# Kernel optimization log

Hardware: AMD Instinct MI355X
Metric: run time of the kernel (lower is better)

Reference implementation:

```python
import jax, jax.numpy as jnp
import numpy as np

SEQ, B, D_IN, D_H = 512, 64, 512, 512


def setup_inputs() -> dict:
    key = jax.random.key(0)
    ks = jax.random.split(key, 5)
    s = 1.0 / np.sqrt(D_IN + D_H)
    inp = {
        "inputs": jax.random.normal(ks[0], (SEQ, B, D_IN), dtype=jnp.float32),
        "W_f": jax.random.normal(ks[1], (D_H, D_IN + D_H), dtype=jnp.float32) * s,
        "b_f": jnp.zeros((D_H,), jnp.float32),
        "W_i": jax.random.normal(ks[2], (D_H, D_IN + D_H), dtype=jnp.float32) * s,
        "b_i": jnp.zeros((D_H,), jnp.float32),
        "W_g": jax.random.normal(ks[3], (D_H, D_IN + D_H), dtype=jnp.float32) * s,
        "b_g": jnp.zeros((D_H,), jnp.float32),
        "W_o": jax.random.normal(ks[4], (D_H, D_IN + D_H), dtype=jnp.float32) * s,
        "b_o": jnp.zeros((D_H,), jnp.float32),
    }
    return inp


def reference(inputs, W_f, b_f, W_i, b_i, W_g, b_g, W_o, b_o):
    # inputs: [seq, batch, d_in]; states start at zeros (module default)
    B_ = inputs.shape[1]
    h0 = jnp.zeros((B_, D_H), inputs.dtype)
    c0 = jnp.zeros((B_, D_H), inputs.dtype)

    def step(carry, x_t):
        hx, cx = carry
        combined = jnp.concatenate([x_t, hx], axis=1)  # [B, d_in+d_h]
        f = jax.nn.sigmoid(combined @ W_f.T + b_f)
        i = jax.nn.sigmoid(combined @ W_i.T + b_i)
        g = jnp.tanh(combined @ W_g.T + b_g)
        o = jax.nn.sigmoid(combined @ W_o.T + b_o)
        cx = f * cx + i * g
        hx = o * jnp.tanh(cx)
        return (hx, cx), hx

    (hx, cx), stacked = jax.lax.scan(step, (h0, c0), inputs)
    return stacked, hx, cx
```

## Files before the change

kernel.cpp:

```cpp
#include <hip/hip_runtime.h>

#define SEQ   512
#define BATCH 64
#define DIN   512
#define DH    512
#define KTOT  1024
#define NWG   128
#define NTH   256
#define HBUF_BYTES 65536

#define FLAGS_BYTES 65536
#define HBASE_OFF   65536
#define XBF_OFF     (HBASE_OFF + 512 * HBUF_BYTES)
#define XBF_BYTES   ((size_t)SEQ * 4 * 16 * 1024)
#define WS_MODE1    ((size_t)HBASE_OFF + 511 * HBUF_BYTES)
#define WS_MODE2    ((size_t)XBF_OFF + XBF_BYTES)
#define FLAG_STRIDE 1

typedef __attribute__((ext_vector_type(8))) short short8;
typedef __attribute__((ext_vector_type(4))) float f32x4;

__device__ __forceinline__ float tanh_fast(float v) {
    const float e = __expf(2.0f * v);
    return 1.0f - 2.0f / (e + 1.0f);
}

__device__ __forceinline__ unsigned int f2bf(float f) {
    unsigned int u = __float_as_uint(f);
    return (u + 0x7fffu + ((u >> 16) & 1u)) >> 16;
}

__device__ __forceinline__ short8 cvt8(float4 lo, float4 hi) {
    short8 r;
    r[0] = (short)f2bf(lo.x); r[1] = (short)f2bf(lo.y);
    r[2] = (short)f2bf(lo.z); r[3] = (short)f2bf(lo.w);
    r[4] = (short)f2bf(hi.x); r[5] = (short)f2bf(hi.y);
    r[6] = (short)f2bf(hi.z); r[7] = (short)f2bf(hi.w);
    return r;
}

__device__ __forceinline__ unsigned int ld_flag(const unsigned int* p) {
    return __hip_atomic_load(p, __ATOMIC_RELAXED, __HIP_MEMORY_SCOPE_AGENT);
}
__device__ __forceinline__ void st_flag(unsigned int* p, unsigned int v) {
    __hip_atomic_store(p, v, __ATOMIC_RELAXED, __HIP_MEMORY_SCOPE_AGENT);
}
__device__ __forceinline__ unsigned long long ld_h_sc1(const unsigned long long* p) {
    return __hip_atomic_load(p, __ATOMIC_RELAXED, __HIP_MEMORY_SCOPE_AGENT);
}
__device__ __forceinline__ void st_h(unsigned long long* p, unsigned long long v) {
    __hip_atomic_store(p, v, __ATOMIC_RELAXED, __HIP_MEMORY_SCOPE_AGENT);
}

__global__ __launch_bounds__(256)
void xconv(const float* __restrict__ x, unsigned short* __restrict__ xbf)
{
    const int gid = blockIdx.x * 256 + threadIdx.x;
    const int l   = gid & 63;
    const int kt  = (gid >> 6) & 15;
    const int mtt = (gid >> 10) & 3;
    const int t   = gid >> 12;
    const float* src = x + ((size_t)t * BATCH + mtt * 16 + (l & 15)) * DIN
                         + kt * 32 + (l >> 4) * 8;
    *(short8*)(xbf + (size_t)gid * 8) =
        cvt8(*(const float4*)src, *(const float4*)(src + 4));
}

template <int MODE>
__global__ __launch_bounds__(NTH, 1)
void lstm_mfma(const float* __restrict__ x,
               const unsigned short* __restrict__ xbf,
               const float* __restrict__ Wf, const float* __restrict__ bfp,
               const float* __restrict__ Wi, const float* __restrict__ bip,
               const float* __restrict__ Wg, const float* __restrict__ bgp,
               const float* __restrict__ Wo, const float* __restrict__ bop,
               float* __restrict__ out,
               unsigned int* __restrict__ ws_u32)
{
    const int tid = threadIdx.x;
    const int l   = tid & 63;
    const int mt  = tid >> 6;
    const int wg  = blockIdx.x;
    const int j0  = wg * 4;

    const int n    = l & 15;
    const int khi  = l >> 4;
    const bool isg = (khi == 2);

    unsigned int* const flags = ws_u32;
    char* const hbase = (char*)ws_u32 + HBASE_OFF;

    const float* Wn = (n < 8) ? ((n < 4) ? Wf : Wi) : ((n < 12) ? Wg : Wo);
    const float* wrow = Wn + (size_t)(j0 + (n & 3)) * KTOT + khi * 8;
    short8 Bfr[32];
    #pragma unroll
    for (int kt = 0; kt < 32; ++kt) {
        Bfr[kt] = cvt8(*(const float4*)(wrow + kt * 32),
                       *(const float4*)(wrow + kt * 32 + 4));
    }
    const float* bptr = (khi == 0) ? bfp : (khi == 1) ? bip : (khi == 2) ? bgp : bop;
    const float4 bias4 = *(const float4*)(bptr + j0);

    float cst0 = 0.f, cst1 = 0.f, cst2 = 0.f, cst3 = 0.f;

    float* const hx_out = out + (size_t)SEQ * BATCH * DH;
    float* const cx_out = hx_out + (size_t)BATCH * DH;

    const int kth         = wg >> 3;
    const int lane_f_base = ((wg & 7) >> 1) << 4;
    const int half8       = (wg & 1) * 8;

    const unsigned int* const f0p = flags + ((size_t)mt * 128 + l) * FLAG_STRIDE;
    const unsigned int* const f1p = f0p + (size_t)64 * FLAG_STRIDE;
    unsigned int* const my_flag = flags + ((size_t)mt * 128 + wg) * FLAG_STRIDE;

    const float*  xrow_base = x + (size_t)(mt * 16 + (l & 15)) * DIN + khi * 8;
    const short8* xbf_base  = (const short8*)xbf + (size_t)mt * 16 * 64 + l;

    for (int t = 0; t < SEQ; ++t) {
        f32x4 acc_a = {0.f, 0.f, 0.f, 0.f};
        f32x4 acc_b = {0.f, 0.f, 0.f, 0.f};

        if (MODE == 2) {
            const short8* xp = xbf_base + (size_t)t * 4096;
            #pragma unroll
            for (int kt = 0; kt < 16; kt += 2) {
                acc_a = __builtin_amdgcn_mfma_f32_16x16x32_bf16(Bfr[kt], xp[kt * 64],
                                                                acc_a, 0, 0, 0);
                acc_b = __builtin_amdgcn_mfma_f32_16x16x32_bf16(Bfr[kt + 1], xp[(kt + 1) * 64],
                                                                acc_b, 0, 0, 0);
            }
        } else {
            const float* xr = xrow_base + (size_t)t * BATCH * DIN;
            #pragma unroll
            for (int kt = 0; kt < 16; kt += 2) {
                const short8 a0 = cvt8(*(const float4*)(xr + kt * 32),
                                       *(const float4*)(xr + kt * 32 + 4));
                const short8 a1 = cvt8(*(const float4*)(xr + (kt + 1) * 32),
                                       *(const float4*)(xr + (kt + 1) * 32 + 4));
                acc_a = __builtin_amdgcn_mfma_f32_16x16x32_bf16(Bfr[kt], a0, acc_a, 0, 0, 0);
                acc_b = __builtin_amdgcn_mfma_f32_16x16x32_bf16(Bfr[kt + 1], a1, acc_b, 0, 0, 0);
            }
        }

        if (t > 0) {
            const unsigned int target = (unsigned int)t;
            for (;;) {
                const unsigned int fa = ld_flag(f0p);
                const unsigned int fb = ld_flag(f1p);
                if (__all(fa >= target && fb >= target)) break;
                __builtin_amdgcn_s_sleep(1);
            }
            asm volatile("" ::: "memory");

            if (MODE == 0) {
                const unsigned long long* hp =
                    (const unsigned long long*)(hbase + ((t & 1) ^ 1) * HBUF_BYTES)
                    + ((size_t)(mt * 16) * 64 + l) * 2;
                #pragma unroll
                for (int kt = 0; kt < 16; kt += 2) {
                    union { unsigned long long u[2]; short8 v; } U0, U1;
                    U0.u[0] = ld_h_sc1(hp + kt * 128);
                    U0.u[1] = ld_h_sc1(hp + kt * 128 + 1);
                    U1.u[0] = ld_h_sc1(hp + (kt + 1) * 128);
                    U1.u[1] = ld_h_sc1(hp + (kt + 1) * 128 + 1);
                    acc_a = __builtin_amdgcn_mfma_f32_16x16x32_bf16(Bfr[16 + kt], U0.v,
                                                                    acc_a, 0, 0, 0);
                    acc_b = __builtin_amdgcn_mfma_f32_16x16x32_bf16(Bfr[17 + kt], U1.v,
                                                                    acc_b, 0, 0, 0);
                }
            } else {
                const uint4* hp = (const uint4*)(hbase + (size_t)(t - 1) * HBUF_BYTES)
                                  + ((size_t)(mt * 16) * 64 + l);
                uint4 hv[16];
                #pragma unroll
                for (int kt = 0; kt < 16; ++kt) hv[kt] = hp[kt * 64];
                #pragma unroll
                for (int kt = 0; kt < 16; kt += 2) {
                    union { uint4 u; short8 v; } U0, U1;
                    U0.u = hv[kt]; U1.u = hv[kt + 1];
                    acc_a = __builtin_amdgcn_mfma_f32_16x16x32_bf16(Bfr[16 + kt], U0.v,
                                                                    acc_a, 0, 0, 0);
                    acc_b = __builtin_amdgcn_mfma_f32_16x16x32_bf16(Bfr[17 + kt], U1.v,
                                                                    acc_b, 0, 0, 0);
                }
            }
        }

        float aq0, aq1, aq2, aq3;
        {
            const float m = isg ? 2.0f : 1.0f;
            const float p0 = acc_a[0] + acc_b[0] + bias4.x;
            const float p1 = acc_a[1] + acc_b[1] + bias4.y;
            const float p2 = acc_a[2] + acc_b[2] + bias4.z;
            const float p3 = acc_a[3] + acc_b[3] + bias4.w;
            const float y0 = 1.0f / (1.0f + __expf(-m * p0));
            const float y1 = 1.0f / (1.0f + __expf(-m * p1));
            const float y2 = 1.0f / (1.0f + __expf(-m * p2));
            const float y3 = 1.0f / (1.0f + __expf(-m * p3));
            aq0 = isg ? 2.0f * y0 - 1.0f : y0;
            aq1 = isg ? 2.0f * y1 - 1.0f : y1;
            aq2 = isg ? 2.0f * y2 - 1.0f : y2;
            aq3 = isg ? 2.0f * y3 - 1.0f : y3;
        }
        const float i0 = __shfl_xor(aq0, 16), g0 = __shfl_xor(aq0, 32), o0 = __shfl_xor(aq0, 48);
        const float i1 = __shfl_xor(aq1, 16), g1 = __shfl_xor(aq1, 32), o1 = __shfl_xor(aq1, 48);
        const float i2 = __shfl_xor(aq2, 16), g2 = __shfl_xor(aq2, 32), o2 = __shfl_xor(aq2, 48);
        const float i3 = __shfl_xor(aq3, 16), g3 = __shfl_xor(aq3, 32), o3 = __shfl_xor(aq3, 48);

        const bool active = (l < 16);
        float hq0 = 0.f, hq1 = 0.f, hq2 = 0.f, hq3 = 0.f;

        if (active) {
            cst0 = fmaf(aq0, cst0, i0 * g0); hq0 = o0 * tanh_fast(cst0);
            cst1 = fmaf(aq1, cst1, i1 * g1); hq1 = o1 * tanh_fast(cst1);
            cst2 = fmaf(aq2, cst2, i2 * g2); hq2 = o2 * tanh_fast(cst2);
            cst3 = fmaf(aq3, cst3, i3 * g3); hq3 = o3 * tanh_fast(cst3);

            if (t < SEQ - 1) {
                const unsigned long long pk =
                    (unsigned long long)(f2bf(hq0) | (f2bf(hq1) << 16))
                    | ((unsigned long long)(f2bf(hq2) | (f2bf(hq3) << 16)) << 32);
                char* const wb = (MODE == 0) ? hbase + (t & 1) * HBUF_BYTES
                                             : hbase + (size_t)t * HBUF_BYTES;
                unsigned long long* hp_w = (unsigned long long*)
                    (wb + (((size_t)(mt * 16 + kth) * 64
                            + (lane_f_base | l)) << 4) + half8);
                st_h(hp_w, pk);
            }
        }

        if (t < SEQ - 1) {
            asm volatile("s_waitcnt vmcnt(0)" ::: "memory");
            if (l == 0) st_flag(my_flag, (unsigned int)(t + 1));
        }

        if (active) {
            const int b = mt * 16 + l;
            const float4 ov = make_float4(hq0, hq1, hq2, hq3);
            *(float4*)(out + ((size_t)t * BATCH + b) * DH + j0) = ov;
            if (t == SEQ - 1) {
                *(float4*)(hx_out + (size_t)b * DH + j0) = ov;
                *(float4*)(cx_out + (size_t)b * DH + j0) =
                    make_float4(cst0, cst1, cst2, cst3);
            }
        }
    }
}

extern "C" void kernel_launch(void* const* d_in, const int* in_sizes, int n_in,
                              void* d_out, int out_size, void* d_ws, size_t ws_size,
                              hipStream_t stream)
{
    const float* x  = (const float*)d_in[0];
    const float* Wf = (const float*)d_in[1];
    const float* bf = (const float*)d_in[2];
    const float* Wi = (const float*)d_in[3];
    const float* bi = (const float*)d_in[4];
    const float* Wg = (const float*)d_in[5];
    const float* bg = (const float*)d_in[6];
    const float* Wo = (const float*)d_in[7];
    const float* bo = (const float*)d_in[8];
    float* out = (float*)d_out;

    hipMemsetAsync(d_ws, 0, FLAGS_BYTES, stream);

    unsigned int* wsp = (unsigned int*)d_ws;
    if (ws_size >= WS_MODE2) {
        unsigned short* xbf = (unsigned short*)((char*)d_ws + XBF_OFF);
        xconv<<<SEQ * 4 * 16 * 64 / 256, 256, 0, stream>>>(x, xbf);
        lstm_mfma<2><<<NWG, NTH, 0, stream>>>(x, xbf, Wf, bf, Wi, bi,
                                              Wg, bg, Wo, bo, out, wsp);
    } else if (ws_size >= WS_MODE1) {
        lstm_mfma<1><<<NWG, NTH, 0, stream>>>(x, nullptr, Wf, bf, Wi, bi,
                                              Wg, bg, Wo, bo, out, wsp);
    } else {
        lstm_mfma<0><<<NWG, NTH, 0, stream>>>(x, nullptr, Wf, bf, Wi, bi,
                                              Wg, bg, Wo, bo, out, wsp);
    }
}
```

Measured before the change: 2.149 ms.

## Drop bf16 x precompute, use producer-contiguous h layout and paired flag loads

```diff
diff --git a/kernel.cpp b/kernel.cpp
--- a/kernel.cpp
+++ b/kernel.cpp
@@ -11,25 +11,19 @@
 
 #define FLAGS_BYTES 65536
 #define HBASE_OFF   65536
-#define XBF_OFF     (HBASE_OFF + 512 * HBUF_BYTES)
-#define XBF_BYTES   ((size_t)SEQ * 4 * 16 * 1024)
-#define WS_MODE1    ((size_t)HBASE_OFF + 511 * HBUF_BYTES)
-#define WS_MODE2    ((size_t)XBF_OFF + XBF_BYTES)
-#define FLAG_STRIDE 1
 
 typedef __attribute__((ext_vector_type(8))) short short8;
 typedef __attribute__((ext_vector_type(4))) float f32x4;
+typedef __attribute__((ext_vector_type(4))) unsigned int u32x4;
 
 __device__ __forceinline__ float tanh_fast(float v) {
     const float e = __expf(2.0f * v);
     return 1.0f - 2.0f / (e + 1.0f);
 }
-
 __device__ __forceinline__ unsigned int f2bf(float f) {
     unsigned int u = __float_as_uint(f);
     return (u + 0x7fffu + ((u >> 16) & 1u)) >> 16;
 }
-
 __device__ __forceinline__ short8 cvt8(float4 lo, float4 hi) {
     short8 r;
     r[0] = (short)f2bf(lo.x); r[1] = (short)f2bf(lo.y);
@@ -38,38 +32,18 @@
     r[6] = (short)f2bf(hi.z); r[7] = (short)f2bf(hi.w);
     return r;
 }
-
-__device__ __forceinline__ unsigned int ld_flag(const unsigned int* p) {
+__device__ __forceinline__ unsigned long long ld_flag64(const unsigned long long* p) {
     return __hip_atomic_load(p, __ATOMIC_RELAXED, __HIP_MEMORY_SCOPE_AGENT);
 }
 __device__ __forceinline__ void st_flag(unsigned int* p, unsigned int v) {
     __hip_atomic_store(p, v, __ATOMIC_RELAXED, __HIP_MEMORY_SCOPE_AGENT);
 }
-__device__ __forceinline__ unsigned long long ld_h_sc1(const unsigned long long* p) {
-    return __hip_atomic_load(p, __ATOMIC_RELAXED, __HIP_MEMORY_SCOPE_AGENT);
-}
 __device__ __forceinline__ void st_h(unsigned long long* p, unsigned long long v) {
     __hip_atomic_store(p, v, __ATOMIC_RELAXED, __HIP_MEMORY_SCOPE_AGENT);
 }
 
-__global__ __launch_bounds__(256)
-void xconv(const float* __restrict__ x, unsigned short* __restrict__ xbf)
-{
-    const int gid = blockIdx.x * 256 + threadIdx.x;
-    const int l   = gid & 63;
-    const int kt  = (gid >> 6) & 15;
-    const int mtt = (gid >> 10) & 3;
-    const int t   = gid >> 12;
-    const float* src = x + ((size_t)t * BATCH + mtt * 16 + (l & 15)) * DIN
-                         + kt * 32 + (l >> 4) * 8;
-    *(short8*)(xbf + (size_t)gid * 8) =
-        cvt8(*(const float4*)src, *(const float4*)(src + 4));
-}
-
-template <int MODE>
 __global__ __launch_bounds__(NTH, 1)
 void lstm_mfma(const float* __restrict__ x,
-               const unsigned short* __restrict__ xbf,
                const float* __restrict__ Wf, const float* __restrict__ bfp,
                const float* __restrict__ Wi, const float* __restrict__ bip,
                const float* __restrict__ Wg, const float* __restrict__ bgp,
@@ -102,35 +76,22 @@
     const float4 bias4 = *(const float4*)(bptr + j0);
 
     float cst0 = 0.f, cst1 = 0.f, cst2 = 0.f, cst3 = 0.f;
-
     float* const hx_out = out + (size_t)SEQ * BATCH * DH;
     float* const cx_out = hx_out + (size_t)BATCH * DH;
 
-    const int kth         = wg >> 3;
-    const int lane_f_base = ((wg & 7) >> 1) << 4;
-    const int half8       = (wg & 1) * 8;
-
-    const unsigned int* const f0p = flags + ((size_t)mt * 128 + l) * FLAG_STRIDE;
-    const unsigned int* const f1p = f0p + (size_t)64 * FLAG_STRIDE;
-    unsigned int* const my_flag = flags + ((size_t)mt * 128 + wg) * FLAG_STRIDE;
-
-    const float*  xrow_base = x + (size_t)(mt * 16 + (l & 15)) * DIN + khi * 8;
-    const short8* xbf_base  = (const short8*)xbf + (size_t)mt * 16 * 64 + l;
+    const size_t prod_base = ((size_t)(mt * 128 + wg)) << 7;
+
+    const unsigned long long* const fpair =
+        (const unsigned long long*)(flags + (size_t)mt * 128) + l;
+    unsigned int* const my_flag = flags + (size_t)mt * 128 + wg;
+
+    const float* xrow_base = x + (size_t)(mt * 16 + n) * DIN + khi * 8;
 
     for (int t = 0; t < SEQ; ++t) {
         f32x4 acc_a = {0.f, 0.f, 0.f, 0.f};
         f32x4 acc_b = {0.f, 0.f, 0.f, 0.f};
 
-        if (MODE == 2) {
-            const short8* xp = xbf_base + (size_t)t * 4096;
-            #pragma unroll
-            for (int kt = 0; kt < 16; kt += 2) {
-                acc_a = __builtin_amdgcn_mfma_f32_16x16x32_bf16(Bfr[kt], xp[kt * 64],
-                                                                acc_a, 0, 0, 0);
-                acc_b = __builtin_amdgcn_mfma_f32_16x16x32_bf16(Bfr[kt + 1], xp[(kt + 1) * 64],
-                                                                acc_b, 0, 0, 0);
-            }
-        } else {
+        {
             const float* xr = xrow_base + (size_t)t * BATCH * DIN;
             #pragma unroll
             for (int kt = 0; kt < 16; kt += 2) {
@@ -146,44 +107,40 @@
         if (t > 0) {
             const unsigned int target = (unsigned int)t;
             for (;;) {
-                const unsigned int fa = ld_flag(f0p);
-                const unsigned int fb = ld_flag(f1p);
+                const unsigned long long fp = ld_flag64(fpair);
+                const unsigned int fa = (unsigned int)fp;
+                const unsigned int fb = (unsigned int)(fp >> 32);
                 if (__all(fa >= target && fb >= target)) break;
                 __builtin_amdgcn_s_sleep(1);
             }
             asm volatile("" ::: "memory");
 
-            if (MODE == 0) {
-                const unsigned long long* hp =
-                    (const unsigned long long*)(hbase + ((t & 1) ^ 1) * HBUF_BYTES)
-                    + ((size_t)(mt * 16) * 64 + l) * 2;
-                #pragma unroll
-                for (int kt = 0; kt < 16; kt += 2) {
-                    union { unsigned long long u[2]; short8 v; } U0, U1;
-                    U0.u[0] = ld_h_sc1(hp + kt * 128);
-                    U0.u[1] = ld_h_sc1(hp + kt * 128 + 1);
-                    U1.u[0] = ld_h_sc1(hp + (kt + 1) * 128);
-                    U1.u[1] = ld_h_sc1(hp + (kt + 1) * 128 + 1);
-                    acc_a = __builtin_amdgcn_mfma_f32_16x16x32_bf16(Bfr[16 + kt], U0.v,
-                                                                    acc_a, 0, 0, 0);
-                    acc_b = __builtin_amdgcn_mfma_f32_16x16x32_bf16(Bfr[17 + kt], U1.v,
-                                                                    acc_b, 0, 0, 0);
-                }
-            } else {
-                const uint4* hp = (const uint4*)(hbase + (size_t)(t - 1) * HBUF_BYTES)
-                                  + ((size_t)(mt * 16) * 64 + l);
-                uint4 hv[16];
-                #pragma unroll
-                for (int kt = 0; kt < 16; ++kt) hv[kt] = hp[kt * 64];
-                #pragma unroll
-                for (int kt = 0; kt < 16; kt += 2) {
-                    union { uint4 u; short8 v; } U0, U1;
-                    U0.u = hv[kt]; U1.u = hv[kt + 1];
-                    acc_a = __builtin_amdgcn_mfma_f32_16x16x32_bf16(Bfr[16 + kt], U0.v,
-                                                                    acc_a, 0, 0, 0);
-                    acc_b = __builtin_amdgcn_mfma_f32_16x16x32_bf16(Bfr[17 + kt], U1.v,
-                                                                    acc_b, 0, 0, 0);
-                }
+            const char* hb = hbase + (size_t)(t - 1) * HBUF_BYTES
+                           + ((size_t)(mt * 128) << 7)
+                           + ((size_t)khi << 8)
+                           + ((size_t)n << 3);
+            unsigned long long q0[16], q1[16];
+            #pragma unroll
+            for (int kt = 0; kt < 16; ++kt) {
+                const char* pc = hb + ((size_t)kt << 10);
+                q0[kt] = *(const unsigned long long*)pc;
+                q1[kt] = *(const unsigned long long*)(pc + 128);
+            }
+            #pragma unroll
+            for (int kt = 0; kt < 16; kt += 2) {
+                union { u32x4 u; short8 v; } U0, U1;
+                U0.u[0] = (unsigned int)q0[kt];
+                U0.u[1] = (unsigned int)(q0[kt] >> 32);
+                U0.u[2] = (unsigned int)q1[kt];
+                U0.u[3] = (unsigned int)(q1[kt] >> 32);
+                U1.u[0] = (unsigned int)q0[kt + 1];
+                U1.u[1] = (unsigned int)(q0[kt + 1] >> 32);
+                U1.u[2] = (unsigned int)q1[kt + 1];
+                U1.u[3] = (unsigned int)(q1[kt + 1] >> 32);
+                acc_a = __builtin_amdgcn_mfma_f32_16x16x32_bf16(Bfr[16 + kt], U0.v,
+                                                                acc_a, 0, 0, 0);
+                acc_b = __builtin_amdgcn_mfma_f32_16x16x32_bf16(Bfr[17 + kt], U1.v,
+                                                                acc_b, 0, 0, 0);
             }
         }
 
@@ -221,11 +178,8 @@
                 const unsigned long long pk =
                     (unsigned long long)(f2bf(hq0) | (f2bf(hq1) << 16))
                     | ((unsigned long long)(f2bf(hq2) | (f2bf(hq3) << 16)) << 32);
-                char* const wb = (MODE == 0) ? hbase + (t & 1) * HBUF_BYTES
-                                             : hbase + (size_t)t * HBUF_BYTES;
                 unsigned long long* hp_w = (unsigned long long*)
-                    (wb + (((size_t)(mt * 16 + kth) * 64
-                            + (lane_f_base | l)) << 4) + half8);
+                    (hbase + (size_t)t * HBUF_BYTES + prod_base + ((size_t)l << 3));
                 st_h(hp_w, pk);
             }
         }
@@ -263,19 +217,8 @@
     const float* bo = (const float*)d_in[8];
     float* out = (float*)d_out;
 
-    hipMemsetAsync(d_ws, 0, FLAGS_BYTES, stream);
-
-    unsigned int* wsp = (unsigned int*)d_ws;
-    if (ws_size >= WS_MODE2) {
-        unsigned short* xbf = (unsigned short*)((char*)d_ws + XBF_OFF);
-        xconv<<<SEQ * 4 * 16 * 64 / 256, 256, 0, stream>>>(x, xbf);
-        lstm_mfma<2><<<NWG, NTH, 0, stream>>>(x, xbf, Wf, bf, Wi, bi,
-                                              Wg, bg, Wo, bo, out, wsp);
-    } else if (ws_size >= WS_MODE1) {
-        lstm_mfma<1><<<NWG, NTH, 0, stream>>>(x, nullptr, Wf, bf, Wi, bi,
-                                              Wg, bg, Wo, bo, out, wsp);
-    } else {
-        lstm_mfma<0><<<NWG, NTH, 0, stream>>>(x, nullptr, Wf, bf, Wi, bi,
-                                              Wg, bg, Wo, bo, out, wsp);
-    }
-}
+    (void)hipMemsetAsync(d_ws, 0, FLAGS_BYTES, stream);
+
+    lstm_mfma<<<NWG, NTH, 0, stream>>>(x, Wf, bf, Wi, bi, Wg, bg, Wo, bo,
+                                       out, (unsigned int*)d_ws);
+}
```

Result: slower. 3.217 ms (+49.7%).
